# Performance work log

Hardware: AMD Instinct MI355X
Metric: run time of the kernel (lower is better)

## Reference

```python
import jax, jax.numpy as jnp
import numpy as np

N_NODES = 50000
N_EDGES = 800000
D_IN = 256
D_HID = 512


def setup_inputs() -> dict:
    key = jax.random.key(0)
    k1, k2, k3, k4 = jax.random.split(key, 4)
    x = jax.random.normal(k1, (N_NODES, D_IN), dtype=jnp.float32)
    edge_index = jax.random.randint(k2, (2, N_EDGES), 0, N_NODES, dtype=jnp.int64)
    # SAGEConv params: lin_l (neighbor branch, with bias), lin_r (root branch, no bias)
    W_l = jax.random.normal(k3, (D_IN, D_HID), dtype=jnp.float32) * (1.0 / np.sqrt(D_IN))
    W_r = jax.random.normal(k4, (D_IN, D_HID), dtype=jnp.float32) * (1.0 / np.sqrt(D_IN))
    b = jnp.zeros((D_HID,), dtype=jnp.float32)
    return {"x": x, "edge_index": edge_index, "W_l": W_l, "W_r": W_r, "b": b}


def reference(x, edge_index, W_l, W_r, b):
    # SAGEConv forward: out_i = W_l @ mean_{j in N(i)} x_j + b + W_r @ x_i
    # PyG flow 'source_to_target': messages from edge_index[0] aggregated at edge_index[1]
    src = edge_index[0]
    dst = edge_index[1]
    n = x.shape[0]
    agg = jax.ops.segment_sum(x[src], dst, num_segments=n)          # [N, D_IN]
    cnt = jax.ops.segment_sum(jnp.ones_like(dst, dtype=x.dtype), dst, num_segments=n)
    mean = agg / jnp.maximum(cnt, 1.0)[:, None]                      # isolated nodes -> 0
    out = mean @ W_l + b + x @ W_r                                   # [N, D_HID]
    return out
```

## Files before the change

### kernel.cpp

```cpp
#include <hip/hip_runtime.h>

#define N_NODES 50000
#define N_EDGES 800000
#define D_IN    256
#define D_HID   512
#define NBLK    196

typedef __attribute__((ext_vector_type(8))) short bf16x8;
typedef __attribute__((ext_vector_type(4))) float f32x4;

constexpr size_t OFF_FLAG  = 0;
constexpr size_t OFF_EDGES = 256;
constexpr size_t OFF_BHT   = OFF_EDGES;
constexpr size_t OFF_BLT   = OFF_BHT   + 524288;
constexpr size_t OFF_CNT   = OFF_EDGES + 6400000;
constexpr size_t OFF_OFFS  = OFF_CNT   + 200192;
constexpr size_t OFF_CUR   = OFF_OFFS  + 200448;
constexpr size_t OFF_BSUM  = OFF_CUR;
constexpr size_t OFF_BOFF  = OFF_CUR   + 1024;
constexpr size_t OFF_SORT  = OFF_CUR   + 200192;
constexpr size_t OFF_MEAN  = OFF_SORT  + 3200000;

__device__ inline unsigned bf16_rne_bits(float f) {
    unsigned u = __float_as_uint(f);
    return (u + 0x7fffu + ((u >> 16) & 1u)) >> 16;
}

__global__ void detect_kernel(const unsigned int* __restrict__ ei, int* __restrict__ flag) {
    __shared__ int any;
    if (threadIdx.x == 0) any = 0;
    __syncthreads();
    int local = 0;
    for (int i = threadIdx.x; i < 4096; i += blockDim.x)
        local |= (ei[2 * i + 1] != 0u);
    if (local) any = 1;
    __syncthreads();
    if (threadIdx.x == 0) *flag = any ? 0 : 1;
}

__global__ void convert_hist_kernel(const void* __restrict__ ei, const int* __restrict__ flag,
                                    int* __restrict__ edges32, int* __restrict__ cnt) {
    int i = blockIdx.x * blockDim.x + threadIdx.x;
    if (i >= 2 * N_EDGES) return;
    int v;
    if (*flag) v = (int)((const long long*)ei)[i];
    else       v = ((const int*)ei)[i];
    edges32[i] = v;
    if (i >= N_EDGES) atomicAdd(&cnt[v], 1);
}

__global__ void scan1_kernel(const int* __restrict__ cnt, int* __restrict__ offs,
                             int* __restrict__ bsum) {
    __shared__ int wsum[4];
    const int tid = threadIdx.x, lane = tid & 63, wid = tid >> 6;
    const int idx = blockIdx.x * 256 + tid;
    int v = (idx < N_NODES) ? cnt[idx] : 0;
    int x = v;
    #pragma unroll
    for (int d = 1; d < 64; d <<= 1) {
        int y = __shfl_up(x, d);
        if (lane >= d) x += y;
    }
    if (lane == 63) wsum[wid] = x;
    __syncthreads();
    int wpre = 0;
    for (int w = 0; w < wid; ++w) wpre += wsum[w];
    if (idx < N_NODES) offs[idx] = x - v + wpre;
    if (tid == 255) bsum[blockIdx.x] = wsum[0] + wsum[1] + wsum[2] + wsum[3];
}

__global__ void scan2_kernel(const int* __restrict__ bsum, int* __restrict__ boff,
                             int* __restrict__ offs) {
    __shared__ int wsum[4];
    const int tid = threadIdx.x, lane = tid & 63, wid = tid >> 6;
    int v = (tid < NBLK) ? bsum[tid] : 0;
    int x = v;
    #pragma unroll
    for (int d = 1; d < 64; d <<= 1) {
        int y = __shfl_up(x, d);
        if (lane >= d) x += y;
    }
    if (lane == 63) wsum[wid] = x;
    __syncthreads();
    int wpre = 0;
    for (int w = 0; w < wid; ++w) wpre += wsum[w];
    if (tid < NBLK) boff[tid] = x - v + wpre;
    if (tid == 255) offs[N_NODES] = wsum[0] + wsum[1] + wsum[2] + wsum[3];
}

__global__ void scan3_kernel(int* __restrict__ offs, const int* __restrict__ boff) {
    int idx = blockIdx.x * 256 + threadIdx.x;
    if (idx < N_NODES) offs[idx] += boff[blockIdx.x];
}

__global__ void scatter_kernel(const int* __restrict__ src, const int* __restrict__ dst,
                               const int* __restrict__ offs, int* __restrict__ cursor,
                               int* __restrict__ sorted_src) {
    int e = blockIdx.x * blockDim.x + threadIdx.x;
    if (e >= N_EDGES) return;
    int d = dst[e];
    int p = offs[d] + atomicAdd(&cursor[d], 1);
    sorted_src[p] = src[e];
}

__global__ void agg_kernel(const float* __restrict__ x, const int* __restrict__ offs,
                           const int* __restrict__ sorted_src, float* __restrict__ mean) {
    int gw = (blockIdx.x * blockDim.x + threadIdx.x) >> 6;
    int lane = threadIdx.x & 63;
    if (gw >= N_NODES) return;
    int beg = __builtin_amdgcn_readfirstlane(offs[gw]);
    int end = __builtin_amdgcn_readfirstlane(offs[gw + 1]);
    float4 a0 = make_float4(0.f,0.f,0.f,0.f), a1 = a0, a2 = a0, a3 = a0;
    int k = beg;
    for (; k + 4 <= end; k += 4) {
        int s0 = __builtin_amdgcn_readfirstlane(sorted_src[k]);
        int s1 = __builtin_amdgcn_readfirstlane(sorted_src[k + 1]);
        int s2 = __builtin_amdgcn_readfirstlane(sorted_src[k + 2]);
        int s3 = __builtin_amdgcn_readfirstlane(sorted_src[k + 3]);
        float4 v0 = *reinterpret_cast<const float4*>(x + (size_t)s0 * D_IN + lane * 4);
        float4 v1 = *reinterpret_cast<const float4*>(x + (size_t)s1 * D_IN + lane * 4);
        float4 v2 = *reinterpret_cast<const float4*>(x + (size_t)s2 * D_IN + lane * 4);
        float4 v3 = *reinterpret_cast<const float4*>(x + (size_t)s3 * D_IN + lane * 4);
        a0.x += v0.x; a0.y += v0.y; a0.z += v0.z; a0.w += v0.w;
        a1.x += v1.x; a1.y += v1.y; a1.z += v1.z; a1.w += v1.w;
        a2.x += v2.x; a2.y += v2.y; a2.z += v2.z; a2.w += v2.w;
        a3.x += v3.x; a3.y += v3.y; a3.z += v3.z; a3.w += v3.w;
    }
    for (; k < end; ++k) {
        int s0 = __builtin_amdgcn_readfirstlane(sorted_src[k]);
        float4 v0 = *reinterpret_cast<const float4*>(x + (size_t)s0 * D_IN + lane * 4);
        a0.x += v0.x; a0.y += v0.y; a0.z += v0.z; a0.w += v0.w;
    }
    int c = end - beg;
    float inv = (c > 0) ? (1.0f / (float)c) : 0.0f;
    float4 o;
    o.x = (a0.x + a1.x + a2.x + a3.x) * inv;
    o.y = (a0.y + a1.y + a2.y + a3.y) * inv;
    o.z = (a0.z + a1.z + a2.z + a3.z) * inv;
    o.w = (a0.w + a1.w + a2.w + a3.w) * inv;
    *reinterpret_cast<float4*>(mean + (size_t)gw * D_IN + lane * 4) = o;
}

__global__ void prepw_kernel(const float* __restrict__ Wl, const float* __restrict__ Wr,
                             unsigned short* __restrict__ BhT, unsigned short* __restrict__ BlT) {
    int idx = blockIdx.x * blockDim.x + threadIdx.x;
    if (idx >= 512 * 512) return;
    int n = idx >> 9, k = idx & 511;
    float v = (k < 256) ? Wl[(size_t)k * D_HID + n] : Wr[(size_t)(k - 256) * D_HID + n];
    unsigned u = __float_as_uint(v);
    unsigned hi_aligned = (u + 0x7fffu + ((u >> 16) & 1u)) & 0xffff0000u;
    float hf = __uint_as_float(hi_aligned);
    float lo = v - hf;
    BhT[idx] = (unsigned short)(hi_aligned >> 16);
    BlT[idx] = (unsigned short)bf16_rne_bits(lo);
}

#define GBM 128
#define GBN 128
#define GBK 32

__device__ inline int lds_slot(int r, int g) { return r * 4 + (((r >> 1) & 3) ^ g); }

__global__ __launch_bounds__(256, 2) void gemm_mfma(
        const float* __restrict__ mean, const float* __restrict__ x,
        const unsigned short* __restrict__ BhT, const unsigned short* __restrict__ BlT,
        const float* __restrict__ bias, float* __restrict__ out) {
    __shared__ __align__(16) unsigned short Ah_s[GBM * GBK];
    __shared__ __align__(16) unsigned short Al_s[GBM * GBK];
    __shared__ __align__(16) unsigned short Bh_s[GBN * GBK];
    __shared__ __align__(16) unsigned short Bl_s[GBN * GBK];

    const int tid  = threadIdx.x;
    const int lane = tid & 63, wave = tid >> 6;
    const int wr = wave >> 1, wc = wave & 1;
    const int mtile = blockIdx.x >> 2;
    const int ntile = blockIdx.x & 3;
    const int row0 = mtile * GBM, col0 = ntile * GBN;

    const int ar  = tid >> 1;
    const int ach = tid & 1;
    const int agrow = row0 + ar;
    const bool aok = (agrow < N_NODES);

    const int fr = lane & 15, fg = lane >> 4;

    f32x4 acc[4][4];
    #pragma unroll
    for (int i = 0; i < 4; ++i)
        #pragma unroll
        for (int j = 0; j < 4; ++j) acc[i][j] = (f32x4)0.f;

    for (int k0 = 0; k0 < 512; k0 += GBK) {
        {
            const int k0c = k0 + ach * 16;
            float f[16];
            if (aok) {
                const float* asrc = (k0c < 256)
                    ? (mean + (size_t)agrow * D_IN + k0c)
                    : (x    + (size_t)agrow * D_IN + (k0c - 256));
                float4 v0 = *reinterpret_cast<const float4*>(asrc + 0);
                float4 v1 = *reinterpret_cast<const float4*>(asrc + 4);
                float4 v2 = *reinterpret_cast<const float4*>(asrc + 8);
                float4 v3 = *reinterpret_cast<const float4*>(asrc + 12);
                f[0]=v0.x; f[1]=v0.y; f[2]=v0.z; f[3]=v0.w;
                f[4]=v1.x; f[5]=v1.y; f[6]=v1.z; f[7]=v1.w;
                f[8]=v2.x; f[9]=v2.y; f[10]=v2.z; f[11]=v2.w;
                f[12]=v3.x; f[13]=v3.y; f[14]=v3.z; f[15]=v3.w;
            } else {
                #pragma unroll
                for (int e = 0; e < 16; ++e) f[e] = 0.f;
            }
            unsigned h[16], l[16];
            #pragma unroll
            for (int e = 0; e < 16; ++e) {
                unsigned u = __float_as_uint(f[e]);
                unsigned ha = (u + 0x7fffu + ((u >> 16) & 1u)) & 0xffff0000u;
                h[e] = ha;
                float lo = f[e] - __uint_as_float(ha);
                l[e] = bf16_rne_bits(lo);
            }
            uint4 hv0, hv1, lv0, lv1;
            hv0.x = (h[1] & 0xffff0000u)  | (h[0] >> 16);
            hv0.y = (h[3] & 0xffff0000u)  | (h[2] >> 16);
            hv0.z = (h[5] & 0xffff0000u)  | (h[4] >> 16);
            hv0.w = (h[7] & 0xffff0000u)  | (h[6] >> 16);
            hv1.x = (h[9] & 0xffff0000u)  | (h[8] >> 16);
            hv1.y = (h[11] & 0xffff0000u) | (h[10] >> 16);
            hv1.z = (h[13] & 0xffff0000u) | (h[12] >> 16);
            hv1.w = (h[15] & 0xffff0000u) | (h[14] >> 16);
            lv0.x = (l[1] << 16) | l[0];
            lv0.y = (l[3] << 16) | l[2];
            lv0.z = (l[5] << 16) | l[4];
            lv0.w = (l[7] << 16) | l[6];
            lv1.x = (l[9] << 16) | l[8];
            lv1.y = (l[11] << 16) | l[10];
            lv1.z = (l[13] << 16) | l[12];
            lv1.w = (l[15] << 16) | l[14];
            const int g0 = 2 * ach, g1 = 2 * ach + 1;
            *reinterpret_cast<uint4*>(&Ah_s[lds_slot(ar, g0) * 8]) = hv0;
            *reinterpret_cast<uint4*>(&Ah_s[lds_slot(ar, g1) * 8]) = hv1;
            *reinterpret_cast<uint4*>(&Al_s[lds_slot(ar, g0) * 8]) = lv0;
            *reinterpret_cast<uint4*>(&Al_s[lds_slot(ar, g1) * 8]) = lv1;
        }
        #pragma unroll
        for (int i = 0; i < 2; ++i) {
            int s = i * 256 + tid;
            int br = s >> 2, bg = s & 3;
            size_t goff = (size_t)(col0 + br) * 512 + k0 + bg * 8;
            uint4 hb = *reinterpret_cast<const uint4*>(BhT + goff);
            uint4 lb = *reinterpret_cast<const uint4*>(BlT + goff);
            *reinterpret_cast<uint4*>(&Bh_s[lds_slot(br, bg) * 8]) = hb;
            *reinterpret_cast<uint4*>(&Bl_s[lds_slot(br, bg) * 8]) = lb;
        }
        __syncthreads();

        bf16x8 ah[4], al[4], bh[4], bl[4];
        #pragma unroll
        for (int m = 0; m < 4; ++m) {
            int r = wr * 64 + m * 16 + fr;
            ah[m] = *reinterpret_cast<const bf16x8*>(&Ah_s[lds_slot(r, fg) * 8]);
            al[m] = *reinterpret_cast<const bf16x8*>(&Al_s[lds_slot(r, fg) * 8]);
        }
        #pragma unroll
        for (int n = 0; n < 4; ++n) {
            int r = wc * 64 + n * 16 + fr;
            bh[n] = *reinterpret_cast<const bf16x8*>(&Bh_s[lds_slot(r, fg) * 8]);
            bl[n] = *reinterpret_cast<const bf16x8*>(&Bl_s[lds_slot(r, fg) * 8]);
        }
        #pragma unroll
        for (int m = 0; m < 4; ++m)
            #pragma unroll
            for (int n = 0; n < 4; ++n) {
                acc[m][n] = __builtin_amdgcn_mfma_f32_16x16x32_bf16(ah[m], bh[n], acc[m][n], 0, 0, 0);
                acc[m][n] = __builtin_amdgcn_mfma_f32_16x16x32_bf16(al[m], bh[n], acc[m][n], 0, 0, 0);
                acc[m][n] = __builtin_amdgcn_mfma_f32_16x16x32_bf16(ah[m], bl[n], acc[m][n], 0, 0, 0);
            }
        __syncthreads();
    }

    float bv[4];
    #pragma unroll
    for (int n = 0; n < 4; ++n) bv[n] = bias[col0 + wc * 64 + n * 16 + fr];
    #pragma unroll
    for (int m = 0; m < 4; ++m) {
        #pragma unroll
        for (int v = 0; v < 4; ++v) {
            int grow = row0 + wr * 64 + m * 16 + fg * 4 + v;
            if (grow < N_NODES) {
                size_t base = (size_t)grow * D_HID + col0 + wc * 64 + fr;
                #pragma unroll
                for (int n = 0; n < 4; ++n)
                    out[base + n * 16] = acc[m][n][v] + bv[n];
            }
        }
    }
}

extern "C" void kernel_launch(void* const* d_in, const int* in_sizes, int n_in,
                              void* d_out, int out_size, void* d_ws, size_t ws_size,
                              hipStream_t stream) {
    const float* x    = (const float*)d_in[0];
    const void*  ei   = d_in[1];
    const float* Wl   = (const float*)d_in[2];
    const float* Wr   = (const float*)d_in[3];
    const float* bias = (const float*)d_in[4];
    float* out = (float*)d_out;

    char* ws = (char*)d_ws;
    int*   flag       = (int*)(ws + OFF_FLAG);
    int*   edges32    = (int*)(ws + OFF_EDGES);
    int*   src32      = edges32;
    int*   dst32      = edges32 + N_EDGES;
    int*   cnt        = (int*)(ws + OFF_CNT);
    int*   offs       = (int*)(ws + OFF_OFFS);
    int*   cursor     = (int*)(ws + OFF_CUR);
    int*   bsum       = (int*)(ws + OFF_BSUM);
    int*   boff       = (int*)(ws + OFF_BOFF);
    int*   sorted_src = (int*)(ws + OFF_SORT);
    float* mean       = (float*)(ws + OFF_MEAN);
    unsigned short* BhT = (unsigned short*)(ws + OFF_BHT);
    unsigned short* BlT = (unsigned short*)(ws + OFF_BLT);

    hipMemsetAsync(cnt, 0, N_NODES * sizeof(int), stream);

    detect_kernel<<<1, 256, 0, stream>>>((const unsigned int*)ei, flag);
    convert_hist_kernel<<<(2 * N_EDGES + 255) / 256, 256, 0, stream>>>(ei, flag, edges32, cnt);
    scan1_kernel<<<NBLK, 256, 0, stream>>>(cnt, offs, bsum);
    scan2_kernel<<<1, 256, 0, stream>>>(bsum, boff, offs);
    scan3_kernel<<<NBLK, 256, 0, stream>>>(offs, boff);
    hipMemsetAsync(cursor, 0, N_NODES * sizeof(int), stream);
    scatter_kernel<<<(N_EDGES + 255) / 256, 256, 0, stream>>>(src32, dst32, offs, cursor, sorted_src);
    prepw_kernel<<<(512 * 512 + 255) / 256, 256, 0, stream>>>(Wl, Wr, BhT, BlT);
    agg_kernel<<<(N_NODES * 64 + 255) / 256, 256, 0, stream>>>(x, offs, sorted_src, mean);

    const int mtiles = (N_NODES + GBM - 1) / GBM;
    gemm_mfma<<<mtiles * 4, 256, 0, stream>>>(mean, x, BhT, BlT, bias, out);
}
```

Measured before the change: 435.9 us.

## Gather neighbor features in fp16 and store mean as fp16

Adds a pass that converts x to fp16. The aggregation kernel now gathers half-width rows, with two edges in flight per wave (one per half-wave), accumulates in fp32, and combines the halves with a shuffle. The mean is written as fp16 and the GEMM reads the fp16 mean for the neighbor branch. This halves gather and mean traffic, at the cost of an extra conversion pass over x and reduced precision in the neighbor features.

```diff
diff --git a/kernel.cpp b/kernel.cpp
--- a/kernel.cpp
+++ b/kernel.cpp
@@ -8,6 +8,7 @@
 
 typedef __attribute__((ext_vector_type(8))) short bf16x8;
 typedef __attribute__((ext_vector_type(4))) float f32x4;
+typedef __attribute__((ext_vector_type(8))) _Float16 f16x8;
 
 constexpr size_t OFF_FLAG  = 0;
 constexpr size_t OFF_EDGES = 256;
@@ -19,7 +20,8 @@
 constexpr size_t OFF_BSUM  = OFF_CUR;
 constexpr size_t OFF_BOFF  = OFF_CUR   + 1024;
 constexpr size_t OFF_SORT  = OFF_CUR   + 200192;
-constexpr size_t OFF_MEAN  = OFF_SORT  + 3200000;
+constexpr size_t OFF_XH    = OFF_SORT  + 3200000;
+constexpr size_t OFF_M16   = OFF_XH    + 25600000;
 
 __device__ inline unsigned bf16_rne_bits(float f) {
     unsigned u = __float_as_uint(f);
@@ -49,6 +51,17 @@
     if (i >= N_EDGES) atomicAdd(&cnt[v], 1);
 }
 
+__global__ void prepx_kernel(const float* __restrict__ x, f16x8* __restrict__ xh) {
+    int i = blockIdx.x * 256 + threadIdx.x;
+    if (i >= N_NODES * D_IN / 8) return;
+    const float4* s = reinterpret_cast<const float4*>(x + (size_t)i * 8);
+    float4 a = s[0], b = s[1];
+    f16x8 o;
+    o[0] = (_Float16)a.x; o[1] = (_Float16)a.y; o[2] = (_Float16)a.z; o[3] = (_Float16)a.w;
+    o[4] = (_Float16)b.x; o[5] = (_Float16)b.y; o[6] = (_Float16)b.z; o[7] = (_Float16)b.w;
+    xh[i] = o;
+}
+
 __global__ void scan1_kernel(const int* __restrict__ cnt, int* __restrict__ offs,
                              int* __restrict__ bsum) {
     __shared__ int wsum[4];
@@ -103,42 +116,48 @@
     sorted_src[p] = src[e];
 }
 
-__global__ void agg_kernel(const float* __restrict__ x, const int* __restrict__ offs,
-                           const int* __restrict__ sorted_src, float* __restrict__ mean) {
+__global__ void agg_kernel(const f16x8* __restrict__ xh, const int* __restrict__ offs,
+                           const int* __restrict__ sorted_src, f16x8* __restrict__ m16) {
     int gw = (blockIdx.x * blockDim.x + threadIdx.x) >> 6;
     int lane = threadIdx.x & 63;
     if (gw >= N_NODES) return;
     int beg = __builtin_amdgcn_readfirstlane(offs[gw]);
     int end = __builtin_amdgcn_readfirstlane(offs[gw + 1]);
-    float4 a0 = make_float4(0.f,0.f,0.f,0.f), a1 = a0, a2 = a0, a3 = a0;
+    const int half = lane >> 5, cb = lane & 31;
+    float a0[8] = {0,0,0,0,0,0,0,0}, a1[8] = {0,0,0,0,0,0,0,0};
     int k = beg;
     for (; k + 4 <= end; k += 4) {
-        int s0 = __builtin_amdgcn_readfirstlane(sorted_src[k]);
-        int s1 = __builtin_amdgcn_readfirstlane(sorted_src[k + 1]);
-        int s2 = __builtin_amdgcn_readfirstlane(sorted_src[k + 2]);
-        int s3 = __builtin_amdgcn_readfirstlane(sorted_src[k + 3]);
-        float4 v0 = *reinterpret_cast<const float4*>(x + (size_t)s0 * D_IN + lane * 4);
-        float4 v1 = *reinterpret_cast<const float4*>(x + (size_t)s1 * D_IN + lane * 4);
-        float4 v2 = *reinterpret_cast<const float4*>(x + (size_t)s2 * D_IN + lane * 4);
-        float4 v3 = *reinterpret_cast<const float4*>(x + (size_t)s3 * D_IN + lane * 4);
-        a0.x += v0.x; a0.y += v0.y; a0.z += v0.z; a0.w += v0.w;
-        a1.x += v1.x; a1.y += v1.y; a1.z += v1.z; a1.w += v1.w;
-        a2.x += v2.x; a2.y += v2.y; a2.z += v2.z; a2.w += v2.w;
-        a3.x += v3.x; a3.y += v3.y; a3.z += v3.z; a3.w += v3.w;
-    }
-    for (; k < end; ++k) {
-        int s0 = __builtin_amdgcn_readfirstlane(sorted_src[k]);
-        float4 v0 = *reinterpret_cast<const float4*>(x + (size_t)s0 * D_IN + lane * 4);
-        a0.x += v0.x; a0.y += v0.y; a0.z += v0.z; a0.w += v0.w;
+        int s0 = sorted_src[k + half];
+        int s1 = sorted_src[k + 2 + half];
+        f16x8 v0 = xh[(size_t)s0 * 32 + cb];
+        f16x8 v1 = xh[(size_t)s1 * 32 + cb];
+        #pragma unroll
+        for (int j = 0; j < 8; ++j) { a0[j] += (float)v0[j]; a1[j] += (float)v1[j]; }
+    }
+    if (k + 2 <= end) {
+        int s0 = sorted_src[k + half];
+        f16x8 v0 = xh[(size_t)s0 * 32 + cb];
+        #pragma unroll
+        for (int j = 0; j < 8; ++j) a0[j] += (float)v0[j];
+        k += 2;
+    }
+    if (k < end && half == 0) {
+        int s0 = sorted_src[k];
+        f16x8 v0 = xh[(size_t)s0 * 32 + cb];
+        #pragma unroll
+        for (int j = 0; j < 8; ++j) a0[j] += (float)v0[j];
     }
     int c = end - beg;
     float inv = (c > 0) ? (1.0f / (float)c) : 0.0f;
-    float4 o;
-    o.x = (a0.x + a1.x + a2.x + a3.x) * inv;
-    o.y = (a0.y + a1.y + a2.y + a3.y) * inv;
-    o.z = (a0.z + a1.z + a2.z + a3.z) * inv;
-    o.w = (a0.w + a1.w + a2.w + a3.w) * inv;
-    *reinterpret_cast<float4*>(mean + (size_t)gw * D_IN + lane * 4) = o;
+    float tot[8];
+    #pragma unroll
+    for (int j = 0; j < 8; ++j) tot[j] = a0[j] + a1[j];
+    #pragma unroll
+    for (int j = 0; j < 8; ++j) tot[j] += __shfl(tot[j], lane ^ 32, 64);
+    f16x8 o;
+    #pragma unroll
+    for (int j = 0; j < 8; ++j) o[j] = (_Float16)(tot[j] * inv);
+    if (half == 0) m16[(size_t)gw * 32 + cb] = o;
 }
 
 __global__ void prepw_kernel(const float* __restrict__ Wl, const float* __restrict__ Wr,
@@ -162,7 +181,7 @@
 __device__ inline int lds_slot(int r, int g) { return r * 4 + (((r >> 1) & 3) ^ g); }
 
 __global__ __launch_bounds__(256, 2) void gemm_mfma(
-        const float* __restrict__ mean, const float* __restrict__ x,
+        const _Float16* __restrict__ mean16, const float* __restrict__ x,
         const unsigned short* __restrict__ BhT, const unsigned short* __restrict__ BlT,
         const float* __restrict__ bias, float* __restrict__ out) {
     __shared__ __align__(16) unsigned short Ah_s[GBM * GBK];
@@ -195,17 +214,23 @@
             const int k0c = k0 + ach * 16;
             float f[16];
             if (aok) {
-                const float* asrc = (k0c < 256)
-                    ? (mean + (size_t)agrow * D_IN + k0c)
-                    : (x    + (size_t)agrow * D_IN + (k0c - 256));
-                float4 v0 = *reinterpret_cast<const float4*>(asrc + 0);
-                float4 v1 = *reinterpret_cast<const float4*>(asrc + 4);
-                float4 v2 = *reinterpret_cast<const float4*>(asrc + 8);
-                float4 v3 = *reinterpret_cast<const float4*>(asrc + 12);
-                f[0]=v0.x; f[1]=v0.y; f[2]=v0.z; f[3]=v0.w;
-                f[4]=v1.x; f[5]=v1.y; f[6]=v1.z; f[7]=v1.w;
-                f[8]=v2.x; f[9]=v2.y; f[10]=v2.z; f[11]=v2.w;
-                f[12]=v3.x; f[13]=v3.y; f[14]=v3.z; f[15]=v3.w;
+                if (k0c < 256) {
+                    const f16x8* mp = reinterpret_cast<const f16x8*>(
+                        mean16 + (size_t)agrow * D_IN + k0c);
+                    f16x8 p0 = mp[0], p1 = mp[1];
+                    #pragma unroll
+                    for (int e = 0; e < 8; ++e) { f[e] = (float)p0[e]; f[e + 8] = (float)p1[e]; }
+                } else {
+                    const float* asrc = x + (size_t)agrow * D_IN + (k0c - 256);
+                    float4 v0 = *reinterpret_cast<const float4*>(asrc + 0);
+                    float4 v1 = *reinterpret_cast<const float4*>(asrc + 4);
+                    float4 v2 = *reinterpret_cast<const float4*>(asrc + 8);
+                    float4 v3 = *reinterpret_cast<const float4*>(asrc + 12);
+                    f[0]=v0.x; f[1]=v0.y; f[2]=v0.z; f[3]=v0.w;
+                    f[4]=v1.x; f[5]=v1.y; f[6]=v1.z; f[7]=v1.w;
+                    f[8]=v2.x; f[9]=v2.y; f[10]=v2.z; f[11]=v2.w;
+                    f[12]=v3.x; f[13]=v3.y; f[14]=v3.z; f[15]=v3.w;
+                }
             } else {
                 #pragma unroll
                 for (int e = 0; e < 16; ++e) f[e] = 0.f;
@@ -317,7 +342,8 @@
     int*   bsum       = (int*)(ws + OFF_BSUM);
     int*   boff       = (int*)(ws + OFF_BOFF);
     int*   sorted_src = (int*)(ws + OFF_SORT);
-    float* mean       = (float*)(ws + OFF_MEAN);
+    f16x8* xh         = (f16x8*)(ws + OFF_XH);
+    f16x8* m16        = (f16x8*)(ws + OFF_M16);
     unsigned short* BhT = (unsigned short*)(ws + OFF_BHT);
     unsigned short* BlT = (unsigned short*)(ws + OFF_BLT);
 
@@ -325,14 +351,15 @@
 
     detect_kernel<<<1, 256, 0, stream>>>((const unsigned int*)ei, flag);
     convert_hist_kernel<<<(2 * N_EDGES + 255) / 256, 256, 0, stream>>>(ei, flag, edges32, cnt);
+    prepx_kernel<<<(N_NODES * D_IN / 8 + 255) / 256, 256, 0, stream>>>(x, xh);
     scan1_kernel<<<NBLK, 256, 0, stream>>>(cnt, offs, bsum);
     scan2_kernel<<<1, 256, 0, stream>>>(bsum, boff, offs);
     scan3_kernel<<<NBLK, 256, 0, stream>>>(offs, boff);
     hipMemsetAsync(cursor, 0, N_NODES * sizeof(int), stream);
     scatter_kernel<<<(N_EDGES + 255) / 256, 256, 0, stream>>>(src32, dst32, offs, cursor, sorted_src);
     prepw_kernel<<<(512 * 512 + 255) / 256, 256, 0, stream>>>(Wl, Wr, BhT, BlT);
-    agg_kernel<<<(N_NODES * 64 + 255) / 256, 256, 0, stream>>>(x, offs, sorted_src, mean);
+    agg_kernel<<<(N_NODES * 64 + 255) / 256, 256, 0, stream>>>(xh, offs, sorted_src, m16);
 
     const int mtiles = (N_NODES + GBM - 1) / GBM;
-    gemm_mfma<<<mtiles * 4, 256, 0, stream>>>(mean, x, BhT, BlT, bias, out);
-}
+    gemm_mfma<<<mtiles * 4, 256, 0, stream>>>((const _Float16*)m16, x, BhT, BlT, bias, out);
+}
```

Result: faster. 394.9 us (-9.4%).
